# Performance work log

Hardware: AMD Instinct MI355X
Metric: run time of the kernel (lower is better)

Reference implementation:

```python
import jax, jax.numpy as jnp
import numpy as np

N = 100000       # nodes
E = 50000        # hyperedges
NNZ = 1600000    # incidence pairs
D = 128          # in_channels == heads*out_channels (heads=1)


def setup_inputs() -> dict:
    key = jax.random.key(0)
    k1, k2, k3, k4 = jax.random.split(key, 4)
    X = jax.random.normal(k1, (N, D), dtype=jnp.float32)
    W = jax.random.normal(k2, (D, D), dtype=jnp.float32) * (1.0 / np.sqrt(D))
    eps = jnp.zeros((1,), dtype=jnp.float32)
    vertex = jax.random.randint(k3, (NNZ,), 0, N, dtype=jnp.int32)
    edges = jax.random.randint(k4, (NNZ,), 0, E, dtype=jnp.int32)
    return {"X": X, "W": W, "eps": eps, "vertex": vertex, "edges": edges}


def reference(X, W, eps, vertex, edges):
    # X' = X W  (nn.Linear with no bias)
    Xp = X @ W                                    # [N, D]
    # vertex -> edge gather then scatter-mean (args.first_aggregate='mean')
    Xve = Xp[vertex]                              # [NNZ, D]
    Xe_sum = jax.ops.segment_sum(Xve, edges, num_segments=E)          # [E, D]
    cnt = jax.ops.segment_sum(jnp.ones((Xve.shape[0],), Xve.dtype), edges,
                              num_segments=E)                          # [E]
    Xe = Xe_sum / jnp.maximum(cnt, 1.0)[:, None]  # mean, empty edges -> 0
    # edge -> vertex gather then scatter-sum
    Xev = Xe[edges]                               # [NNZ, D]
    Xv = jax.ops.segment_sum(Xev, vertex, num_segments=N)             # [N, D]
    # GIN residual
    out = (1.0 + eps[0]) * Xp + Xv
    # args.use_norm: row-wise L2 normalize
    nrm = jnp.sqrt(jnp.sum(out * out, axis=-1, keepdims=True))
    out = out / jnp.maximum(nrm, 1e-12)
    return (out, Xe)
```

## Files before the change

### kernel.cpp

```cpp
#include <hip/hip_runtime.h>
#include <hip/hip_bf16.h>

#define NN   100000
#define NE   50000
#define NNZP 1600000
#define DD   128

#define EBK  512
#define NBE  ((NE + EBK - 1) / EBK)
#define VBK  512
#define NBV  ((NN + VBK - 1) / VBK)
#define NBT  (NBE + NBV)
#define CH2  3200
#define NSB  500

typedef __attribute__((ext_vector_type(8))) short bf16x8;
typedef __attribute__((ext_vector_type(4))) float f32x4;
typedef __attribute__((ext_vector_type(2))) unsigned int u32x2;

__device__ __forceinline__ ushort f2bf(float f) {
    __hip_bfloat16 h = __float2bfloat16(f);
    return *reinterpret_cast<ushort*>(&h);
}
__device__ __forceinline__ void accP(u32x2 u, float& ax, float& ay, float& az, float& aw) {
    ax += __uint_as_float(u.x << 16);
    ay += __uint_as_float(u.x & 0xffff0000u);
    az += __uint_as_float(u.y << 16);
    aw += __uint_as_float(u.y & 0xffff0000u);
}
__device__ __forceinline__ u32x2 ldg_u2(const ushort* p) {
    return *reinterpret_cast<const u32x2*>(p);
}

__global__ __launch_bounds__(256) void scatter_count(const int* __restrict__ vertex,
                                                     const int* __restrict__ edges,
                                                     int* __restrict__ blkCnt,
                                                     const float* __restrict__ W,
                                                     ushort* __restrict__ Wt) {
    __shared__ int c[NBT];
    const int t = threadIdx.x;
    if (blockIdx.x >= NSB) {
        int i = (blockIdx.x - NSB) * 256 + t;
        if (i < DD * DD) { int k = i >> 7, n = i & 127; Wt[n * DD + k] = f2bf(W[i]); }
        return;
    }
    for (int i = t; i < NBT; i += 256) c[i] = 0;
    __syncthreads();
    const int base = blockIdx.x * CH2;
    for (int i = t; i < CH2 / 4; i += 256) {
        int4 e4 = *reinterpret_cast<const int4*>(edges + base + i * 4);
        int4 v4 = *reinterpret_cast<const int4*>(vertex + base + i * 4);
        atomicAdd(&c[e4.x >> 9], 1); atomicAdd(&c[e4.y >> 9], 1);
        atomicAdd(&c[e4.z >> 9], 1); atomicAdd(&c[e4.w >> 9], 1);
        atomicAdd(&c[NBE + (v4.x >> 9)], 1); atomicAdd(&c[NBE + (v4.y >> 9)], 1);
        atomicAdd(&c[NBE + (v4.z >> 9)], 1); atomicAdd(&c[NBE + (v4.w >> 9)], 1);
    }
    __syncthreads();
    for (int i = t; i < NBT; i += 256) blkCnt[i * NSB + blockIdx.x] = c[i];
}

__global__ __launch_bounds__(256) void blk_scan(int* __restrict__ blkCnt,
                                                int* __restrict__ gCnt) {
    __shared__ int wsum[4];
    const int t = threadIdx.x;
    int* p = blkCnt + blockIdx.x * NSB;
    int c0 = (2 * t     < NSB) ? p[2 * t]     : 0;
    int c1 = (2 * t + 1 < NSB) ? p[2 * t + 1] : 0;
    int s = c0 + c1;
    int inc = s;
    #pragma unroll
    for (int d = 1; d < 64; d <<= 1) {
        int x = __shfl_up(inc, d, 64);
        if ((t & 63) >= d) inc += x;
    }
    if ((t & 63) == 63) wsum[t >> 6] = inc;
    __syncthreads();
    int wid = t >> 6, wbase = 0;
    #pragma unroll
    for (int w = 0; w < 3; ++w) if (w < wid) wbase += wsum[w];
    int excl = wbase + inc - s;
    if (2 * t     < NSB) p[2 * t]     = excl;
    if (2 * t + 1 < NSB) p[2 * t + 1] = excl + c0;
    if (t == 255) gCnt[blockIdx.x] = wbase + inc;
}

__global__ __launch_bounds__(512) void bucket_scan(const int* __restrict__ gCnt,
                                                   int* __restrict__ eBase,
                                                   int* __restrict__ vBase,
                                                   int* __restrict__ eoff,
                                                   int* __restrict__ voff) {
    __shared__ int sh[512];
    int t = threadIdx.x;
    int v = (t < NBT) ? gCnt[t] : 0;
    sh[t] = v;
    __syncthreads();
    for (int d = 1; d < 512; d <<= 1) {
        int x = (t >= d) ? sh[t - d] : 0;
        __syncthreads();
        sh[t] += x;
        __syncthreads();
    }
    int excl = sh[t] - v;
    if (t < NBE)      eBase[t] = excl;
    else if (t < NBT) vBase[t - NBE] = excl - NNZP;
    if (t == 0) { eBase[NBE] = NNZP; vBase[NBV] = NNZP; eoff[NE] = NNZP; voff[NN] = NNZP; }
}

__global__ __launch_bounds__(256) void scatter_place(const int* __restrict__ vertex,
                                                     const int* __restrict__ edges,
                                                     const int* __restrict__ blkCnt,
                                                     const int* __restrict__ eBase,
                                                     const int* __restrict__ vBase,
                                                     unsigned int* __restrict__ ebuckP,
                                                     unsigned int* __restrict__ vbuckP) {
    __shared__ int cur[NBT];
    const int t = threadIdx.x;
    const int base = blockIdx.x * CH2;
    for (int i = t; i < NBT; i += 256) {
        int rel = blkCnt[i * NSB + blockIdx.x];
        cur[i] = ((i < NBE) ? eBase[i] : vBase[i - NBE]) + rel;
    }
    __syncthreads();
    for (int i = t; i < CH2 / 2; i += 256) {
        int2 e2 = *reinterpret_cast<const int2*>(edges + base + i * 2);
        int2 v2 = *reinterpret_cast<const int2*>(vertex + base + i * 2);
        int pe0 = atomicAdd(&cur[e2.x >> 9], 1);
        ebuckP[pe0] = ((unsigned)(e2.x & 511) << 17) | (unsigned)v2.x;
        int pe1 = atomicAdd(&cur[e2.y >> 9], 1);
        ebuckP[pe1] = ((unsigned)(e2.y & 511) << 17) | (unsigned)v2.y;
        int pv0 = atomicAdd(&cur[NBE + (v2.x >> 9)], 1);
        vbuckP[pv0] = ((unsigned)(v2.x & 511) << 16) | (unsigned)e2.x;
        int pv1 = atomicAdd(&cur[NBE + (v2.y >> 9)], 1);
        vbuckP[pv1] = ((unsigned)(v2.y & 511) << 16) | (unsigned)e2.y;
    }
}

__global__ __launch_bounds__(256) void gemm_mfma(const float* __restrict__ X,
                                                 const ushort* __restrict__ Wt,
                                                 ushort* __restrict__ Xp16) {
    __shared__ char WtL[DD * DD * 2];
    for (int c = threadIdx.x; c < 2048; c += 256) {
        int n = c >> 4, kc = c & 15;
        int dst = (n * 256 + kc * 16) ^ ((n & 7) << 4);
        *reinterpret_cast<int4*>(WtL + dst) = reinterpret_cast<const int4*>(Wt)[c];
    }
    __syncthreads();
    int wave = threadIdx.x >> 6;
    int lane = threadIdx.x & 63;
    int r = lane & 15, half = lane >> 4;
    #pragma unroll
    for (int rt = 0; rt < 2; ++rt) {
        int rowTile = blockIdx.x * 8 + wave * 2 + rt;
        if (rowTile >= NN / 16) break;
        const float* xrow = X + (size_t)(rowTile * 16 + r) * DD;
        f32x4 acc[8];
        #pragma unroll
        for (int nt = 0; nt < 8; ++nt) acc[nt] = (f32x4)(0.f);
        #pragma unroll
        for (int kk = 0; kk < DD; kk += 32) {
            int kbase = kk + half * 8;
            float4 xa = *reinterpret_cast<const float4*>(xrow + kbase);
            float4 xb = *reinterpret_cast<const float4*>(xrow + kbase + 4);
            bf16x8 a;
            a[0] = (short)f2bf(xa.x); a[1] = (short)f2bf(xa.y);
            a[2] = (short)f2bf(xa.z); a[3] = (short)f2bf(xa.w);
            a[4] = (short)f2bf(xb.x); a[5] = (short)f2bf(xb.y);
            a[6] = (short)f2bf(xb.z); a[7] = (short)f2bf(xb.w);
            #pragma unroll
            for (int nt = 0; nt < 8; ++nt) {
                int n = nt * 16 + r;
                int off = (n * 256 + kbase * 2) ^ ((n & 7) << 4);
                bf16x8 b = *reinterpret_cast<const bf16x8*>(WtL + off);
                acc[nt] = __builtin_amdgcn_mfma_f32_16x16x32_bf16(a, b, acc[nt], 0, 0, 0);
            }
        }
        int row0 = rowTile * 16 + half * 4;
        #pragma unroll
        for (int nt = 0; nt < 8; ++nt)
            #pragma unroll
            for (int q = 0; q < 4; ++q)
                Xp16[(size_t)(row0 + q) * DD + nt * 16 + r] = f2bf(acc[nt][q]);
    }
}

__global__ __launch_bounds__(256) void place_buckets2(const unsigned int* __restrict__ ebuckP,
                                                      const unsigned int* __restrict__ vbuckP,
                                                      const int* __restrict__ eBase,
                                                      const int* __restrict__ vBase,
                                                      int* __restrict__ eoff,
                                                      int* __restrict__ voff,
                                                      int* __restrict__ vlist,
                                                      int* __restrict__ elist) {
    __shared__ int cnt[EBK];
    __shared__ int wsum[4];
    const int t = threadIdx.x;
    int b = blockIdx.x;
    const unsigned int* buck; int id0, nid, start, end; int* off; int* lst;
    int sh_amt; unsigned msk;
    if (b < NBE) {
        buck = ebuckP; id0 = b * EBK; nid = min(EBK, NE - id0);
        start = eBase[b]; end = eBase[b + 1]; off = eoff; lst = vlist;
        sh_amt = 17; msk = 0x1FFFFu;
    } else {
        b -= NBE;
        buck = vbuckP; id0 = b * VBK; nid = min(VBK, NN - id0);
        start = vBase[b]; end = vBase[b + 1]; off = voff; lst = elist;
        sh_amt = 16; msk = 0xFFFFu;
    }
    for (int i = t; i < nid; i += 256) cnt[i] = 0;
    __syncthreads();
    for (int i = start + t; i < end; i += 256)
        atomicAdd(&cnt[buck[i] >> sh_amt], 1);
    __syncthreads();
    int c0 = (2 * t     < nid) ? cnt[2 * t]     : 0;
    int c1 = (2 * t + 1 < nid) ? cnt[2 * t + 1] : 0;
    int s = c0 + c1;
    int inc = s;
    #pragma unroll
    for (int d = 1; d < 64; d <<= 1) {
        int x = __shfl_up(inc, d, 64);
        if ((t & 63) >= d) inc += x;
    }
    if ((t & 63) == 63) wsum[t >> 6] = inc;
    __syncthreads();
    int wid = t >> 6, wbase = 0;
    #pragma unroll
    for (int w = 0; w < 3; ++w) if (w < wid) wbase += wsum[w];
    int excl = start + wbase + (inc - s);
    if (2 * t     < nid) off[id0 + 2 * t]     = excl;
    if (2 * t + 1 < nid) off[id0 + 2 * t + 1] = excl + c0;
    __syncthreads();
    if (2 * t     < nid) cnt[2 * t]     = excl;
    if (2 * t + 1 < nid) cnt[2 * t + 1] = excl + c0;
    __syncthreads();
    for (int i = start + t; i < end; i += 256) {
        unsigned p = buck[i];
        lst[atomicAdd(&cnt[p >> sh_amt], 1)] = (int)(p & msk);
    }
}

__global__ __launch_bounds__(256) void edge_gather(const ushort* __restrict__ Xp16,
                                                   const int* __restrict__ eoff,
                                                   const int* __restrict__ vlist,
                                                   float* __restrict__ Xe,
                                                   ushort* __restrict__ Xe16) {
    int e = blockIdx.x * 8 + (threadIdx.x >> 5);
    if (e >= NE) return;
    int lane = threadIdx.x & 31;
    int start = eoff[e], end = eoff[e + 1];
    float ax = 0.f, ay = 0.f, az = 0.f, aw = 0.f;
    int j = start;
    for (; j + 7 < end; j += 8) {
        int v0 = vlist[j],     v1 = vlist[j + 1], v2 = vlist[j + 2], v3 = vlist[j + 3];
        int v4 = vlist[j + 4], v5 = vlist[j + 5], v6 = vlist[j + 6], v7 = vlist[j + 7];
        u32x2 u0 = ldg_u2(Xp16 + (size_t)v0 * DD + lane * 4);
        u32x2 u1 = ldg_u2(Xp16 + (size_t)v1 * DD + lane * 4);
        u32x2 u2 = ldg_u2(Xp16 + (size_t)v2 * DD + lane * 4);
        u32x2 u3 = ldg_u2(Xp16 + (size_t)v3 * DD + lane * 4);
        u32x2 u4 = ldg_u2(Xp16 + (size_t)v4 * DD + lane * 4);
        u32x2 u5 = ldg_u2(Xp16 + (size_t)v5 * DD + lane * 4);
        u32x2 u6 = ldg_u2(Xp16 + (size_t)v6 * DD + lane * 4);
        u32x2 u7 = ldg_u2(Xp16 + (size_t)v7 * DD + lane * 4);
        accP(u0, ax, ay, az, aw); accP(u1, ax, ay, az, aw);
        accP(u2, ax, ay, az, aw); accP(u3, ax, ay, az, aw);
        accP(u4, ax, ay, az, aw); accP(u5, ax, ay, az, aw);
        accP(u6, ax, ay, az, aw); accP(u7, ax, ay, az, aw);
    }
    for (; j < end; ++j) {
        u32x2 u = ldg_u2(Xp16 + (size_t)vlist[j] * DD + lane * 4);
        accP(u, ax, ay, az, aw);
    }
    float inv = 1.0f / fmaxf((float)(end - start), 1.0f);
    f32x4 o; o[0] = ax * inv; o[1] = ay * inv; o[2] = az * inv; o[3] = aw * inv;
    __builtin_nontemporal_store(o, reinterpret_cast<f32x4*>(Xe + (size_t)e * DD + lane * 4));
    ushort4 h;
    h.x = f2bf(o[0]); h.y = f2bf(o[1]); h.z = f2bf(o[2]); h.w = f2bf(o[3]);
    *reinterpret_cast<ushort4*>(Xe16 + (size_t)e * DD + lane * 4) = h;
}

__global__ __launch_bounds__(256) void vertex_gather_out(const ushort* __restrict__ Xp16,
                                                         const ushort* __restrict__ Xe16,
                                                         const int* __restrict__ voff,
                                                         const int* __restrict__ elist,
                                                         const float* __restrict__ eps,
                                                         float* __restrict__ Out) {
    int v = blockIdx.x * 8 + (threadIdx.x >> 5);
    if (v >= NN) return;
    int lane = threadIdx.x & 31;
    int start = voff[v], end = voff[v + 1];
    float ax = 0.f, ay = 0.f, az = 0.f, aw = 0.f;
    int j = start;
    for (; j + 7 < end; j += 8) {
        int e0 = elist[j],     e1 = elist[j + 1], e2 = elist[j + 2], e3 = elist[j + 3];
        int e4 = elist[j + 4], e5 = elist[j + 5], e6 = elist[j + 6], e7 = elist[j + 7];
        u32x2 u0 = ldg_u2(Xe16 + (size_t)e0 * DD + lane * 4);
        u32x2 u1 = ldg_u2(Xe16 + (size_t)e1 * DD + lane * 4);
        u32x2 u2 = ldg_u2(Xe16 + (size_t)e2 * DD + lane * 4);
        u32x2 u3 = ldg_u2(Xe16 + (size_t)e3 * DD + lane * 4);
        u32x2 u4 = ldg_u2(Xe16 + (size_t)e4 * DD + lane * 4);
        u32x2 u5 = ldg_u2(Xe16 + (size_t)e5 * DD + lane * 4);
        u32x2 u6 = ldg_u2(Xe16 + (size_t)e6 * DD + lane * 4);
        u32x2 u7 = ldg_u2(Xe16 + (size_t)e7 * DD + lane * 4);
        accP(u0, ax, ay, az, aw); accP(u1, ax, ay, az, aw);
        accP(u2, ax, ay, az, aw); accP(u3, ax, ay, az, aw);
        accP(u4, ax, ay, az, aw); accP(u5, ax, ay, az, aw);
        accP(u6, ax, ay, az, aw); accP(u7, ax, ay, az, aw);
    }
    for (; j < end; ++j) {
        u32x2 u = ldg_u2(Xe16 + (size_t)elist[j] * DD + lane * 4);
        accP(u, ax, ay, az, aw);
    }
    float g = 1.0f + eps[0];
    u32x2 xp = __builtin_nontemporal_load(
        reinterpret_cast<const u32x2*>(Xp16 + (size_t)v * DD + lane * 4));
    f32x4 o;
    o[0] = fmaf(g, __uint_as_float(xp.x << 16),         ax);
    o[1] = fmaf(g, __uint_as_float(xp.x & 0xffff0000u), ay);
    o[2] = fmaf(g, __uint_as_float(xp.y << 16),         az);
    o[3] = fmaf(g, __uint_as_float(xp.y & 0xffff0000u), aw);
    float ss = o[0] * o[0] + o[1] * o[1] + o[2] * o[2] + o[3] * o[3];
    #pragma unroll
    for (int off = 1; off < 32; off <<= 1) ss += __shfl_xor(ss, off, 64);
    float inv = 1.0f / fmaxf(sqrtf(ss), 1e-12f);
    o[0] *= inv; o[1] *= inv; o[2] *= inv; o[3] *= inv;
    __builtin_nontemporal_store(o, reinterpret_cast<f32x4*>(Out + (size_t)v * DD + lane * 4));
}

extern "C" void kernel_launch(void* const* d_in, const int* in_sizes, int n_in,
                              void* d_out, int out_size, void* d_ws, size_t ws_size,
                              hipStream_t stream) {
    const float* X      = (const float*)d_in[0];
    const float* W      = (const float*)d_in[1];
    const float* eps    = (const float*)d_in[2];
    const int*   vertex = (const int*)d_in[3];
    const int*   edges  = (const int*)d_in[4];

    float* out = (float*)d_out;
    float* Xe  = out + (size_t)NN * DD;

    unsigned int* ebuckP = (unsigned int*)out;
    unsigned int* vbuckP = ebuckP + NNZP;

    ushort* Xp16 = (ushort*)d_ws;
    ushort* Xe16 = Xp16 + (size_t)NN * DD;
    ushort* Wt16 = Xe16 + (size_t)NE * DD;
    int*    eoff = (int*)(Wt16 + DD * DD);
    int*    voff = eoff + NE + 1;
    int*    vlist = voff + NN + 1;
    int*    elist = vlist + NNZP;
    int*    gCnt  = elist + NNZP;
    int*    eBase = gCnt + NBT;
    int*    vBase = eBase + NBE + 1;
    int*    blkCnt = vBase + NBV + 1;

    scatter_count<<<NSB + 64, 256, 0, stream>>>(vertex, edges, blkCnt, W, Wt16);
    gemm_mfma<<<(NN / 16 + 7) / 8, 256, 0, stream>>>(X, Wt16, Xp16);
    blk_scan<<<NBT, 256, 0, stream>>>(blkCnt, gCnt);
    bucket_scan<<<1, 512, 0, stream>>>(gCnt, eBase, vBase, eoff, voff);
    scatter_place<<<NSB, 256, 0, stream>>>(vertex, edges, blkCnt, eBase, vBase, ebuckP, vbuckP);
    place_buckets2<<<NBT, 256, 0, stream>>>(ebuckP, vbuckP, eBase, vBase, eoff, voff, vlist, elist);
    edge_gather<<<NE / 8, 256, 0, stream>>>(Xp16, eoff, vlist, Xe, Xe16);
    vertex_gather_out<<<NN / 8, 256, 0, stream>>>(Xp16, Xe16, voff, elist, eps, out);
}
```

Baseline: 213.5 us.

## Fuse GEMM with scatter placement and fold bucket scan into consumers

Removes the single-block bucket_scan kernel: each block that needs bucket bases now recomputes the exclusive scan over the ~300 bucket counts in shared memory. The GEMM and scatter_place kernels are merged into one launch with disjoint block ranges, so the independent GEMM work can run alongside the scatter placement. This cuts two launches and a serial single-block step, at the cost of redundant per-block scans and a larger shared-memory footprint for placement blocks.

```diff
diff --git a/kernel.cpp b/kernel.cpp
--- a/kernel.cpp
+++ b/kernel.cpp
@@ -13,6 +13,7 @@
 #define NBT  (NBE + NBV)
 #define CH2  3200
 #define NSB  500
+#define NGB  ((NN / 16 + 7) / 8)
 
 typedef __attribute__((ext_vector_type(8))) short bf16x8;
 typedef __attribute__((ext_vector_type(4))) float f32x4;
@@ -30,6 +31,29 @@
 }
 __device__ __forceinline__ u32x2 ldg_u2(const ushort* p) {
     return *reinterpret_cast<const u32x2*>(p);
+}
+
+__device__ __forceinline__ void scan_gcnt(const int* __restrict__ gCnt,
+                                          int* sbase, int* wsum) {
+    const int t = threadIdx.x;
+    int c0 = (2 * t     < NBT) ? gCnt[2 * t]     : 0;
+    int c1 = (2 * t + 1 < NBT) ? gCnt[2 * t + 1] : 0;
+    int s = c0 + c1;
+    int inc = s;
+    #pragma unroll
+    for (int d = 1; d < 64; d <<= 1) {
+        int x = __shfl_up(inc, d, 64);
+        if ((t & 63) >= d) inc += x;
+    }
+    if ((t & 63) == 63) wsum[t >> 6] = inc;
+    __syncthreads();
+    int wid = t >> 6, wbase = 0;
+    #pragma unroll
+    for (int w = 0; w < 3; ++w) if (w < wid) wbase += wsum[w];
+    int excl = wbase + inc - s;
+    if (2 * t     < NBT) sbase[2 * t]     = excl;
+    if (2 * t + 1 < NBT) sbase[2 * t + 1] = excl + c0;
+    __syncthreads();
 }
 
 __global__ __launch_bounds__(256) void scatter_count(const int* __restrict__ vertex,
@@ -60,9 +84,12 @@
 }
 
 __global__ __launch_bounds__(256) void blk_scan(int* __restrict__ blkCnt,
-                                                int* __restrict__ gCnt) {
+                                                int* __restrict__ gCnt,
+                                                int* __restrict__ eoff,
+                                                int* __restrict__ voff) {
     __shared__ int wsum[4];
     const int t = threadIdx.x;
+    if (blockIdx.x == 0 && t == 0) { eoff[NE] = NNZP; voff[NN] = NNZP; }
     int* p = blkCnt + blockIdx.x * NSB;
     int c0 = (2 * t     < NSB) ? p[2 * t]     : 0;
     int c1 = (2 * t + 1 < NSB) ? p[2 * t + 1] : 0;
@@ -84,127 +111,111 @@
     if (t == 255) gCnt[blockIdx.x] = wbase + inc;
 }
 
-__global__ __launch_bounds__(512) void bucket_scan(const int* __restrict__ gCnt,
-                                                   int* __restrict__ eBase,
-                                                   int* __restrict__ vBase,
-                                                   int* __restrict__ eoff,
-                                                   int* __restrict__ voff) {
-    __shared__ int sh[512];
-    int t = threadIdx.x;
-    int v = (t < NBT) ? gCnt[t] : 0;
-    sh[t] = v;
-    __syncthreads();
-    for (int d = 1; d < 512; d <<= 1) {
-        int x = (t >= d) ? sh[t - d] : 0;
+__global__ __launch_bounds__(256) void place_gemm(const int* __restrict__ vertex,
+                                                  const int* __restrict__ edges,
+                                                  const int* __restrict__ blkCnt,
+                                                  const int* __restrict__ gCnt,
+                                                  unsigned int* __restrict__ ebuckP,
+                                                  unsigned int* __restrict__ vbuckP,
+                                                  const float* __restrict__ X,
+                                                  const ushort* __restrict__ Wt,
+                                                  ushort* __restrict__ Xp16) {
+    __shared__ char smem[DD * DD * 2];
+    __shared__ int wsum[4];
+    const int t = threadIdx.x;
+    if (blockIdx.x < NGB) {
+        char* WtL = smem;
+        for (int c = t; c < 2048; c += 256) {
+            int n = c >> 4, kc = c & 15;
+            int dst = (n * 256 + kc * 16) ^ ((n & 7) << 4);
+            *reinterpret_cast<int4*>(WtL + dst) = reinterpret_cast<const int4*>(Wt)[c];
+        }
         __syncthreads();
-        sh[t] += x;
+        int wave = t >> 6;
+        int lane = t & 63;
+        int r = lane & 15, half = lane >> 4;
+        #pragma unroll
+        for (int rt = 0; rt < 2; ++rt) {
+            int rowTile = blockIdx.x * 8 + wave * 2 + rt;
+            if (rowTile >= NN / 16) break;
+            const float* xrow = X + (size_t)(rowTile * 16 + r) * DD;
+            f32x4 acc[8];
+            #pragma unroll
+            for (int nt = 0; nt < 8; ++nt) acc[nt] = (f32x4)(0.f);
+            #pragma unroll
+            for (int kk = 0; kk < DD; kk += 32) {
+                int kbase = kk + half * 8;
+                float4 xa = *reinterpret_cast<const float4*>(xrow + kbase);
+                float4 xb = *reinterpret_cast<const float4*>(xrow + kbase + 4);
+                bf16x8 a;
+                a[0] = (short)f2bf(xa.x); a[1] = (short)f2bf(xa.y);
+                a[2] = (short)f2bf(xa.z); a[3] = (short)f2bf(xa.w);
+                a[4] = (short)f2bf(xb.x); a[5] = (short)f2bf(xb.y);
+                a[6] = (short)f2bf(xb.z); a[7] = (short)f2bf(xb.w);
+                #pragma unroll
+                for (int nt = 0; nt < 8; ++nt) {
+                    int n = nt * 16 + r;
+                    int off = (n * 256 + kbase * 2) ^ ((n & 7) << 4);
+                    bf16x8 b = *reinterpret_cast<const bf16x8*>(WtL + off);
+                    acc[nt] = __builtin_amdgcn_mfma_f32_16x16x32_bf16(a, b, acc[nt], 0, 0, 0);
+                }
+            }
+            int row0 = rowTile * 16 + half * 4;
+            #pragma unroll
+            for (int nt = 0; nt < 8; ++nt)
+                #pragma unroll
+                for (int q = 0; q < 4; ++q)
+                    Xp16[(size_t)(row0 + q) * DD + nt * 16 + r] = f2bf(acc[nt][q]);
+        }
+    } else {
+        const int pb = blockIdx.x - NGB;
+        int* sbase = reinterpret_cast<int*>(smem);
+        int* cur   = sbase + NBT;
+        scan_gcnt(gCnt, sbase, wsum);
+        for (int i = t; i < NBT; i += 256) {
+            int rel = blkCnt[i * NSB + pb];
+            int b = sbase[i] - ((i < NBE) ? 0 : NNZP);
+            cur[i] = b + rel;
+        }
         __syncthreads();
-    }
-    int excl = sh[t] - v;
-    if (t < NBE)      eBase[t] = excl;
-    else if (t < NBT) vBase[t - NBE] = excl - NNZP;
-    if (t == 0) { eBase[NBE] = NNZP; vBase[NBV] = NNZP; eoff[NE] = NNZP; voff[NN] = NNZP; }
-}
-
-__global__ __launch_bounds__(256) void scatter_place(const int* __restrict__ vertex,
-                                                     const int* __restrict__ edges,
-                                                     const int* __restrict__ blkCnt,
-                                                     const int* __restrict__ eBase,
-                                                     const int* __restrict__ vBase,
-                                                     unsigned int* __restrict__ ebuckP,
-                                                     unsigned int* __restrict__ vbuckP) {
-    __shared__ int cur[NBT];
-    const int t = threadIdx.x;
-    const int base = blockIdx.x * CH2;
-    for (int i = t; i < NBT; i += 256) {
-        int rel = blkCnt[i * NSB + blockIdx.x];
-        cur[i] = ((i < NBE) ? eBase[i] : vBase[i - NBE]) + rel;
-    }
-    __syncthreads();
-    for (int i = t; i < CH2 / 2; i += 256) {
-        int2 e2 = *reinterpret_cast<const int2*>(edges + base + i * 2);
-        int2 v2 = *reinterpret_cast<const int2*>(vertex + base + i * 2);
-        int pe0 = atomicAdd(&cur[e2.x >> 9], 1);
-        ebuckP[pe0] = ((unsigned)(e2.x & 511) << 17) | (unsigned)v2.x;
-        int pe1 = atomicAdd(&cur[e2.y >> 9], 1);
-        ebuckP[pe1] = ((unsigned)(e2.y & 511) << 17) | (unsigned)v2.y;
-        int pv0 = atomicAdd(&cur[NBE + (v2.x >> 9)], 1);
-        vbuckP[pv0] = ((unsigned)(v2.x & 511) << 16) | (unsigned)e2.x;
-        int pv1 = atomicAdd(&cur[NBE + (v2.y >> 9)], 1);
-        vbuckP[pv1] = ((unsigned)(v2.y & 511) << 16) | (unsigned)e2.y;
-    }
-}
-
-__global__ __launch_bounds__(256) void gemm_mfma(const float* __restrict__ X,
-                                                 const ushort* __restrict__ Wt,
-                                                 ushort* __restrict__ Xp16) {
-    __shared__ char WtL[DD * DD * 2];
-    for (int c = threadIdx.x; c < 2048; c += 256) {
-        int n = c >> 4, kc = c & 15;
-        int dst = (n * 256 + kc * 16) ^ ((n & 7) << 4);
-        *reinterpret_cast<int4*>(WtL + dst) = reinterpret_cast<const int4*>(Wt)[c];
-    }
-    __syncthreads();
-    int wave = threadIdx.x >> 6;
-    int lane = threadIdx.x & 63;
-    int r = lane & 15, half = lane >> 4;
-    #pragma unroll
-    for (int rt = 0; rt < 2; ++rt) {
-        int rowTile = blockIdx.x * 8 + wave * 2 + rt;
-        if (rowTile >= NN / 16) break;
-        const float* xrow = X + (size_t)(rowTile * 16 + r) * DD;
-        f32x4 acc[8];
-        #pragma unroll
-        for (int nt = 0; nt < 8; ++nt) acc[nt] = (f32x4)(0.f);
-        #pragma unroll
-        for (int kk = 0; kk < DD; kk += 32) {
-            int kbase = kk + half * 8;
-            float4 xa = *reinterpret_cast<const float4*>(xrow + kbase);
-            float4 xb = *reinterpret_cast<const float4*>(xrow + kbase + 4);
-            bf16x8 a;
-            a[0] = (short)f2bf(xa.x); a[1] = (short)f2bf(xa.y);
-            a[2] = (short)f2bf(xa.z); a[3] = (short)f2bf(xa.w);
-            a[4] = (short)f2bf(xb.x); a[5] = (short)f2bf(xb.y);
-            a[6] = (short)f2bf(xb.z); a[7] = (short)f2bf(xb.w);
-            #pragma unroll
-            for (int nt = 0; nt < 8; ++nt) {
-                int n = nt * 16 + r;
-                int off = (n * 256 + kbase * 2) ^ ((n & 7) << 4);
-                bf16x8 b = *reinterpret_cast<const bf16x8*>(WtL + off);
-                acc[nt] = __builtin_amdgcn_mfma_f32_16x16x32_bf16(a, b, acc[nt], 0, 0, 0);
-            }
+        const int base = pb * CH2;
+        for (int i = t; i < CH2 / 2; i += 256) {
+            int2 e2 = *reinterpret_cast<const int2*>(edges + base + i * 2);
+            int2 v2 = *reinterpret_cast<const int2*>(vertex + base + i * 2);
+            int pe0 = atomicAdd(&cur[e2.x >> 9], 1);
+            ebuckP[pe0] = ((unsigned)(e2.x & 511) << 17) | (unsigned)v2.x;
+            int pe1 = atomicAdd(&cur[e2.y >> 9], 1);
+            ebuckP[pe1] = ((unsigned)(e2.y & 511) << 17) | (unsigned)v2.y;
+            int pv0 = atomicAdd(&cur[NBE + (v2.x >> 9)], 1);
+            vbuckP[pv0] = ((unsigned)(v2.x & 511) << 16) | (unsigned)e2.x;
+            int pv1 = atomicAdd(&cur[NBE + (v2.y >> 9)], 1);
+            vbuckP[pv1] = ((unsigned)(v2.y & 511) << 16) | (unsigned)e2.y;
         }
-        int row0 = rowTile * 16 + half * 4;
-        #pragma unroll
-        for (int nt = 0; nt < 8; ++nt)
-            #pragma unroll
-            for (int q = 0; q < 4; ++q)
-                Xp16[(size_t)(row0 + q) * DD + nt * 16 + r] = f2bf(acc[nt][q]);
     }
 }
 
 __global__ __launch_bounds__(256) void place_buckets2(const unsigned int* __restrict__ ebuckP,
                                                       const unsigned int* __restrict__ vbuckP,
-                                                      const int* __restrict__ eBase,
-                                                      const int* __restrict__ vBase,
+                                                      const int* __restrict__ gCnt,
                                                       int* __restrict__ eoff,
                                                       int* __restrict__ voff,
                                                       int* __restrict__ vlist,
                                                       int* __restrict__ elist) {
+    __shared__ int sbase[NBT];
     __shared__ int cnt[EBK];
     __shared__ int wsum[4];
     const int t = threadIdx.x;
+    scan_gcnt(gCnt, sbase, wsum);
     int b = blockIdx.x;
     const unsigned int* buck; int id0, nid, start, end; int* off; int* lst;
     int sh_amt; unsigned msk;
     if (b < NBE) {
         buck = ebuckP; id0 = b * EBK; nid = min(EBK, NE - id0);
-        start = eBase[b]; end = eBase[b + 1]; off = eoff; lst = vlist;
+        start = sbase[b]; end = start + gCnt[b]; off = eoff; lst = vlist;
         sh_amt = 17; msk = 0x1FFFFu;
     } else {
-        b -= NBE;
-        buck = vbuckP; id0 = b * VBK; nid = min(VBK, NN - id0);
-        start = vBase[b]; end = vBase[b + 1]; off = voff; lst = elist;
+        buck = vbuckP; id0 = (b - NBE) * VBK; nid = min(VBK, NN - id0);
+        start = sbase[b] - NNZP; end = start + gCnt[b]; off = voff; lst = elist;
         sh_amt = 16; msk = 0xFFFFu;
     }
     for (int i = t; i < nid; i += 256) cnt[i] = 0;
@@ -349,16 +360,13 @@
     int*    vlist = voff + NN + 1;
     int*    elist = vlist + NNZP;
     int*    gCnt  = elist + NNZP;
-    int*    eBase = gCnt + NBT;
-    int*    vBase = eBase + NBE + 1;
-    int*    blkCnt = vBase + NBV + 1;
+    int*    blkCnt = gCnt + NBT;
 
     scatter_count<<<NSB + 64, 256, 0, stream>>>(vertex, edges, blkCnt, W, Wt16);
-    gemm_mfma<<<(NN / 16 + 7) / 8, 256, 0, stream>>>(X, Wt16, Xp16);
-    blk_scan<<<NBT, 256, 0, stream>>>(blkCnt, gCnt);
-    bucket_scan<<<1, 512, 0, stream>>>(gCnt, eBase, vBase, eoff, voff);
-    scatter_place<<<NSB, 256, 0, stream>>>(vertex, edges, blkCnt, eBase, vBase, ebuckP, vbuckP);
-    place_buckets2<<<NBT, 256, 0, stream>>>(ebuckP, vbuckP, eBase, vBase, eoff, voff, vlist, elist);
+    blk_scan<<<NBT, 256, 0, stream>>>(blkCnt, gCnt, eoff, voff);
+    place_gemm<<<NGB + NSB, 256, 0, stream>>>(vertex, edges, blkCnt, gCnt,
+                                              ebuckP, vbuckP, X, Wt16, Xp16);
+    place_buckets2<<<NBT, 256, 0, stream>>>(ebuckP, vbuckP, gCnt, eoff, voff, vlist, elist);
     edge_gather<<<NE / 8, 256, 0, stream>>>(Xp16, eoff, vlist, Xe, Xe16);
     vertex_gather_out<<<NN / 8, 256, 0, stream>>>(Xp16, Xe16, voff, elist, eps, out);
 }
```

Measured after the change: 209.6 us. About the same (-1.8%).
